# Kernel optimization log

Measured on AMD Instinct MI355X. Metric: run time of the kernel, lower is better.

The kernel has to match this reference:

```python
import jax, jax.numpy as jnp
import numpy as np

B, C, H, W = 8, 512, 64, 64
WS, NH = 8, 16
HD = C // NH
SCALE = float(HD) ** -0.5
L = WS * WS  # tokens per window
BN_EPS = 1e-5


def _rel_index():
    # Swin relative position index, (L, L) int table into (2*WS-1)^2 bias rows
    ch = np.arange(WS)
    coords = np.stack(np.meshgrid(ch, ch, indexing='ij'))  # (2, WS, WS)
    cf = coords.reshape(2, -1)
    rel = cf[:, :, None] - cf[:, None, :]
    rel = rel.transpose(1, 2, 0).copy()
    rel[:, :, 0] += WS - 1
    rel[:, :, 1] += WS - 1
    rel[:, :, 0] *= 2 * WS - 1
    return jnp.asarray(rel.sum(-1))

REL_IDX = _rel_index()


def conv2d(x, w, pad=0, groups=1):
    return jax.lax.conv_general_dilated(
        x, w, (1, 1), [(pad, pad), (pad, pad)],
        feature_group_count=groups,
        dimension_numbers=('NCHW', 'OIHW', 'NCHW'))


def bn(x, g, b):
    # eval-mode BatchNorm with running_mean=0, running_var=1 (fresh init)
    inv = 1.0 / np.sqrt(1.0 + BN_EPS)
    return g[None, :, None, None] * (x * inv) + b[None, :, None, None]


def avgpool(x, kh, kw, ph, pw):
    # torch AvgPool2d: zero padding, count_include_pad=True
    s = jax.lax.reduce_window(x, 0.0, jax.lax.add, (1, 1, kh, kw), (1, 1, 1, 1),
                              ((0, 0), (0, 0), (ph, ph), (pw, pw)))
    return s / (kh * kw)


def setup_inputs() -> dict:
    key = jax.random.key(0)
    ks = jax.random.split(key, 8)
    r = lambda k, s: jax.random.normal(k, s, dtype=jnp.float32) * 0.02
    return {
        'x': jax.random.normal(ks[0], (B, C, H, W), dtype=jnp.float32),
        'w_lc1': r(ks[1], (C, C, 1, 1)),
        'g1': jnp.ones((C,), jnp.float32), 'b1': jnp.zeros((C,), jnp.float32),
        'w_lc2': r(ks[2], (C, C, 3, 3)),
        'g2': jnp.ones((C,), jnp.float32), 'b2': jnp.zeros((C,), jnp.float32),
        'w_qkv': r(ks[3], (3 * C, C, 1, 1)),
        'rel_table': r(ks[4], ((2 * WS - 1) * (2 * WS - 1), NH)),
        'w_dw': r(ks[5], (C, 1, WS, WS)),
        'g3': jnp.ones((C,), jnp.float32), 'b3': jnp.zeros((C,), jnp.float32),
        'w_pw': r(ks[6], (C, C, 1, 1)),
    }


def reference(x, w_lc1, g1, b1, w_lc2, g2, b2, w_qkv, rel_table, w_dw, g3, b3, w_pw):
    # local branch: 1x1 conv+BN  +  3x3 conv+BN
    local = bn(conv2d(x, w_lc1), g1, b1) + bn(conv2d(x, w_lc2, pad=1), g2, b2)

    # H, W divisible by WS -> pad() is a no-op; Hp, Wp = H, W
    hh, ww = H // WS, W // WS
    qkv = conv2d(x, w_qkv)  # (B, 3C, H, W)
    # 'b (qkv h d) (hh ws1) (ww ws2) -> qkv (b hh ww) h (ws1 ws2) d'
    qkv = qkv.reshape(B, 3, NH, HD, hh, WS, ww, WS)
    qkv = qkv.transpose(1, 0, 4, 6, 2, 5, 7, 3).reshape(3, B * hh * ww, NH, L, HD)
    q, k, v = qkv[0], qkv[1], qkv[2]

    dots = jnp.einsum('bhid,bhjd->bhij', q, k) * SCALE  # (Bw, NH, L, L)
    bias = rel_table[REL_IDX]                            # (L, L, NH)
    dots = dots + bias.transpose(2, 0, 1)[None]
    attn = jax.nn.softmax(dots, axis=-1)
    out = jnp.einsum('bhij,bhjd->bhid', attn, v)         # (Bw, NH, L, HD)

    # '(b hh ww) h (ws1 ws2) d -> b (h d) (hh ws1) (ww ws2)'
    out = out.reshape(B, hh, ww, NH, WS, WS, HD)
    out = out.transpose(0, 3, 6, 1, 4, 2, 5).reshape(B, C, H, W)

    ax = avgpool(jnp.pad(out, ((0, 0), (0, 0), (0, 1), (0, 0)), mode='reflect'),
                 WS, 1, WS // 2 - 1, 0)
    ay = avgpool(jnp.pad(out, ((0, 0), (0, 0), (0, 0), (0, 1)), mode='reflect'),
                 1, WS, 0, WS // 2 - 1)
    out = ax + ay + local

    # pad_out + SeparableConvBN(kernel=WS): depthwise conv -> BN -> 1x1 conv
    out = jnp.pad(out, ((0, 0), (0, 0), (0, 1), (0, 1)), mode='reflect')
    out = conv2d(out, w_dw, pad=(WS - 1) // 2, groups=C)
    out = bn(out, g3, b3)
    out = conv2d(out, w_pw)
    return out[:, :, :H, :W]
```

## Files before the change

kernel.cpp:

```cpp
#include <hip/hip_runtime.h>

#define INVBN 0.9999950000374997f
#define ATT_SCALE 0.17677669529663687f

typedef short bf16x8 __attribute__((ext_vector_type(8)));
typedef float f32x4  __attribute__((ext_vector_type(4)));
typedef unsigned short us8v __attribute__((ext_vector_type(8)));

#define AS1C(p) ((const __attribute__((address_space(1))) void*)(p))
#define AS3(p)  ((__attribute__((address_space(3))) void*)(p))

__device__ __forceinline__ float bf2f(unsigned short u) {
    return __uint_as_float(((unsigned)u) << 16);
}
__device__ __forceinline__ unsigned short f2bf(float f) {
    unsigned u = __float_as_uint(f);
    u += 0x7FFFu + ((u >> 16) & 1u);
    return (unsigned short)(u >> 16);
}

__global__ __launch_bounds__(256)
void repack_kernel(const float* __restrict__ W2, const float* __restrict__ W1,
                   const float* __restrict__ Wq, const float* __restrict__ Wp,
                   const float* __restrict__ g1, const float* __restrict__ g2,
                   const float* __restrict__ b1, const float* __restrict__ b2,
                   unsigned short* __restrict__ Wt, unsigned short* __restrict__ WqO,
                   unsigned short* __restrict__ WpO, float* __restrict__ bsum)
{
    int i = blockIdx.x * 256 + threadIdx.x;
    if (i < 512) bsum[i] = b1[i] + b2[i];
    if (i < 786432) WqO[i] = f2bf(Wq[i]);
    if (i < 262144) WpO[i] = f2bf(Wp[i]);
    if (i >= 2359296) return;
    int tap = i / 262144;
    int rem = i - tap * 262144;
    int m   = rem >> 9;
    float v = g2[m] * INVBN * W2[(size_t)rem * 9 + tap];
    if (tap == 4) v = fmaf(g1[m] * INVBN, W1[rem], v);
    Wt[i] = f2bf(v);
}

__global__ __launch_bounds__(256)
void bias_precompute_kernel(const float* __restrict__ RT, float* __restrict__ biasM)
{
    int idx = blockIdx.x * 256 + threadIdx.x;
    int h = idx >> 10, rem = idx & 1023;
    int frag = rem >> 6, lane = rem & 63;
    int fi = frag >> 2, fj = frag & 3;
    int q  = 16 * fj + (lane & 15);
    int kb = 16 * fi + ((lane >> 4) << 2);
    int yi = q >> 3, xi = q & 7;
    float4 o;
    float* op = (float*)&o;
#pragma unroll
    for (int r = 0; r < 4; ++r) {
        int j = kb + r;
        int ridx = (yi - (j >> 3) + 7) * 15 + (xi - (j & 7) + 7);
        op[r] = RT[ridx * 16 + h];
    }
    *(float4*)&biasM[(size_t)idx * 4] = o;
}

__global__ __launch_bounds__(256)
void pad_transpose_kernel(const float* __restrict__ X, unsigned short* __restrict__ XT)
{
    int ph = blockIdx.x;
    int b  = blockIdx.y;
    int t  = threadIdx.x;
    unsigned short* rowbase = XT + ((size_t)b * 4356 + (size_t)ph * 66) * 512;
    uint4 z = make_uint4(0, 0, 0, 0);
    if (ph == 0 || ph == 65) {
        uint4* p4 = (uint4*)rowbase;
        for (int i = t; i < 4224; i += 256) p4[i] = z;
        return;
    }
    if (t < 64)       ((uint4*)rowbase)[t] = z;
    else if (t < 128) ((uint4*)(rowbase + 65 * 512))[t - 64] = z;

    int h = ph - 1;
    __shared__ float tile[64][65];
    const float* xb = X + (size_t)b * 512 * 4096 + h * 64;
    for (int cc = 0; cc < 8; ++cc) {
        int c0 = cc * 64;
        __syncthreads();
#pragma unroll
        for (int i = 0; i < 4; ++i) {
            int cl = i * 16 + (t >> 4);
            int w0 = (t & 15) * 4;
            *(float4*)&tile[cl][w0] =
                *(const float4*)&xb[(size_t)(c0 + cl) * 4096 + w0];
        }
        __syncthreads();
#pragma unroll
        for (int it = 0; it < 2; ++it) {
            int wl = it * 32 + (t >> 3);
            int cs = (t & 7) * 8;
            us8v v;
#pragma unroll
            for (int e = 0; e < 8; ++e) v[e] = f2bf(tile[cs + e][wl]);
            *(us8v*)&rowbase[(size_t)(1 + wl) * 512 + c0 + cs] = v;
        }
    }
}

template<int NTAPS, bool PAD, typename OT>
__global__ __launch_bounds__(256)
void mfma_gemm(const unsigned short* __restrict__ A,
               const unsigned short* __restrict__ Bw,
               const float* __restrict__ bias,
               OT* __restrict__ Out, int M)
{
    __shared__ short As[128 * 64];
    __shared__ short Bs[128 * 64];

    const int t  = threadIdx.x;
    const int n0 = blockIdx.x * 128;
    const int m0 = blockIdx.y * 128;
    const int b  = blockIdx.z;
    const unsigned short* Ab = A + (size_t)b * (PAD ? 4356 * 512 : 4096 * 512);
    OT* Ob = Out + (size_t)b * ((size_t)M * 4096);

    const int trow = t >> 3;
    const int csrc = (t & 7) ^ (trow & 7);
    const unsigned short* aSrc[4];
    const unsigned short* bSrc[4];
#pragma unroll
    for (int i = 0; i < 4; ++i) {
        int r = i * 32 + trow;
        int p = n0 + r;
        if (PAD) {
            int h = p >> 6, w = p & 63;
            aSrc[i] = Ab + ((size_t)((h + 1) * 66 + (w + 1)) * 512 + csrc * 8);
        } else {
            aSrc[i] = Ab + ((size_t)p * 512 + csrc * 8);
        }
        bSrc[i] = Bw + ((size_t)(m0 + r) * 512 + csrc * 8);
    }
    short* aDst = As + (t & 192) * 8;
    short* bDst = Bs + (t & 192) * 8;

    const int lane = t & 63;
    const int wv = t >> 6, wr = wv >> 1, wc = wv & 1;
    const int lrow = lane & 15, lk = lane >> 4;
    int aOff[4][2], bOff[4][2];
#pragma unroll
    for (int f = 0; f < 4; ++f)
#pragma unroll
        for (int kk = 0; kk < 2; ++kk) {
            int ra = wr * 64 + f * 16 + lrow;
            aOff[f][kk] = ra * 64 + ((kk * 4 + lk) ^ (ra & 7)) * 8;
            int rb = wc * 64 + f * 16 + lrow;
            bOff[f][kk] = rb * 64 + ((kk * 4 + lk) ^ (rb & 7)) * 8;
        }

    f32x4 acc[4][4] = {};

#pragma unroll 1
    for (int tap = 0; tap < NTAPS; ++tap) {
        const int dr  = (NTAPS == 9) ? (tap / 3 - 1) : 0;
        const int dsh = (NTAPS == 9) ? (tap % 3 - 1) : 0;
        const int aTapOff = (dr * 66 + dsh) * 512;
        const size_t bTapOff = (size_t)tap * (size_t)M * 512;
#pragma unroll 1
        for (int ks = 0; ks < 8; ++ks) {
            const int k0 = ks * 64;
            __syncthreads();
#pragma unroll
            for (int i = 0; i < 4; ++i) {
                __builtin_amdgcn_global_load_lds(
                    AS1C(aSrc[i] + aTapOff + k0), AS3(aDst + i * 2048), 16, 0, 0);
                __builtin_amdgcn_global_load_lds(
                    AS1C(bSrc[i] + bTapOff + k0), AS3(bDst + i * 2048), 16, 0, 0);
            }
            __syncthreads();
            bf16x8 av[4][2], bv[4][2];
#pragma unroll
            for (int f = 0; f < 4; ++f) {
                av[f][0] = *(const bf16x8*)&As[aOff[f][0]];
                av[f][1] = *(const bf16x8*)&As[aOff[f][1]];
                bv[f][0] = *(const bf16x8*)&Bs[bOff[f][0]];
                bv[f][1] = *(const bf16x8*)&Bs[bOff[f][1]];
            }
#pragma unroll
            for (int kk = 0; kk < 2; ++kk)
#pragma unroll
                for (int fn = 0; fn < 4; ++fn)
#pragma unroll
                    for (int fm = 0; fm < 4; ++fm)
                        acc[fn][fm] = __builtin_amdgcn_mfma_f32_16x16x32_bf16(
                            av[fn][kk], bv[fm][kk], acc[fn][fm], 0, 0, 0);
        }
    }

#pragma unroll
    for (int fm = 0; fm < 4; ++fm) {
        int m = m0 + wc * 64 + fm * 16 + lrow;
        float bv = bias ? bias[m] : 0.f;
        size_t mrow = (size_t)m * 4096;
#pragma unroll
        for (int fn = 0; fn < 4; ++fn) {
            int nb = n0 + wr * 64 + fn * 16 + lk * 4;
            f32x4 a4 = acc[fn][fm];
            if constexpr (sizeof(OT) == 2) {
                ushort4 o;
                o.x = f2bf(a4[0] + bv);
                o.y = f2bf(a4[1] + bv);
                o.z = f2bf(a4[2] + bv);
                o.w = f2bf(a4[3] + bv);
                *(ushort4*)&Ob[mrow + nb] = o;
            } else {
                *(float4*)&Ob[mrow + nb] =
                    make_float4(a4[0] + bv, a4[1] + bv, a4[2] + bv, a4[3] + bv);
            }
        }
    }
}

__global__ __launch_bounds__(256)
void attn_mfma_kernel(const unsigned short* __restrict__ QKV,
                      const float* __restrict__ biasM,
                      float* __restrict__ OutB)
{
    __shared__ short smem[4 * 9216];
    int t = threadIdx.x;
    int wv = t >> 6, lane = t & 63;
    int wing = blockIdx.x >> 2;
    int head = (blockIdx.x & 3) * 4 + wv;
    int b    = blockIdx.y;
    int hhi = wing >> 3, wwi = wing & 7;
    int sp0 = hhi * 512 + wwi * 8;
    int ch0 = head * 32;
    const unsigned short* Qg = QKV + (size_t)b * 1536 * 4096;

    short* Qtm = smem + wv * 9216;
    short* Ktm = Qtm + 2304;
    short* Pq  = Qtm + 4608;

    {
        int d  = lane & 31;
        int rb = lane >> 5;
#pragma unroll
        for (int i = 0; i < 4; ++i) {
            int r = rb + 2 * i;
            us8v q8 = *(const us8v*)&Qg[(size_t)(ch0 + d) * 4096 + sp0 + r * 64];
            us8v k8 = *(const us8v*)&Qg[(size_t)(512 + ch0 + d) * 4096 + sp0 + r * 64];
#pragma unroll
            for (int e = 0; e < 8; ++e) {
                Qtm[(r * 8 + e) * 36 + d] = (short)q8[e];
                Ktm[(r * 8 + e) * 36 + d] = (short)k8[e];
            }
        }
    }

    int lrow = lane & 15, lk = lane >> 4;

    bf16x8 kf[4], qf[4];
#pragma unroll
    for (int f = 0; f < 4; ++f) {
        kf[f] = *(const bf16x8*)&Ktm[(lrow + 16 * f) * 36 + lk * 8];
        qf[f] = *(const bf16x8*)&Qtm[(lrow + 16 * f) * 36 + lk * 8];
    }
    f32x4 s[4][4] = {};
#pragma unroll
    for (int fi = 0; fi < 4; ++fi)
#pragma unroll
        for (int fj = 0; fj < 4; ++fj)
            s[fi][fj] = __builtin_amdgcn_mfma_f32_16x16x32_bf16(
                kf[fi], qf[fj], s[fi][fj], 0, 0, 0);

    const float* bM = biasM + (size_t)head * 4096;
    float rs[4];
#pragma unroll
    for (int fj = 0; fj < 4; ++fj) {
        float v[4][4];
#pragma unroll
        for (int fi = 0; fi < 4; ++fi) {
            float4 bv = *(const float4*)&bM[((fi * 4 + fj) * 64 + lane) * 4];
            const float* bvp = (const float*)&bv;
#pragma unroll
            for (int r = 0; r < 4; ++r)
                v[fi][r] = fmaf(s[fi][fj][r], ATT_SCALE, bvp[r]);
        }
        float m = -1e30f;
#pragma unroll
        for (int fi = 0; fi < 4; ++fi)
#pragma unroll
            for (int r = 0; r < 4; ++r) m = fmaxf(m, v[fi][r]);
        m = fmaxf(m, __shfl_xor(m, 16));
        m = fmaxf(m, __shfl_xor(m, 32));
        float ev[4][4];
        float sum = 0.f;
#pragma unroll
        for (int fi = 0; fi < 4; ++fi)
#pragma unroll
            for (int r = 0; r < 4; ++r) {
                ev[fi][r] = __expf(v[fi][r] - m);
                sum += ev[fi][r];
            }
        sum += __shfl_xor(sum, 16);
        sum += __shfl_xor(sum, 32);
        rs[fj] = 1.f / sum;
#pragma unroll
        for (int fi = 0; fi < 4; ++fi) {
            unsigned p0 = (unsigned)f2bf(ev[fi][0]) | ((unsigned)f2bf(ev[fi][1]) << 16);
            unsigned p1 = (unsigned)f2bf(ev[fi][2]) | ((unsigned)f2bf(ev[fi][3]) << 16);
            *(uint2*)&Pq[(lrow + 16 * fj) * 72 + 16 * fi + lk * 4] = make_uint2(p0, p1);
        }
    }

    f32x4 o[2][4] = {};
#pragma unroll
    for (int ks = 0; ks < 2; ++ks) {
        bf16x8 vf[2], pf[4];
#pragma unroll
        for (int fid = 0; fid < 2; ++fid)
            vf[fid] = *(const bf16x8*)&Qg[(size_t)(1024 + ch0 + 16 * fid + lrow) * 4096
                                          + sp0 + (lk + 4 * ks) * 64];
#pragma unroll
        for (int fjq = 0; fjq < 4; ++fjq)
            pf[fjq] = *(const bf16x8*)&Pq[(lrow + 16 * fjq) * 72 + ks * 32 + lk * 8];
#pragma unroll
        for (int fid = 0; fid < 2; ++fid)
#pragma unroll
            for (int fjq = 0; fjq < 4; ++fjq)
                o[fid][fjq] = __builtin_amdgcn_mfma_f32_16x16x32_bf16(
                    vf[fid], pf[fjq], o[fid][fjq], 0, 0, 0);
    }

    float* Out = OutB + (size_t)b * 512 * 4096;
#pragma unroll
    for (int fjq = 0; fjq < 4; ++fjq) {
        int q  = lrow + 16 * fjq;
        int sp = sp0 + ((q >> 3) << 6) + (q & 7);
        float rr = rs[fjq];
#pragma unroll
        for (int fid = 0; fid < 2; ++fid)
#pragma unroll
            for (int r = 0; r < 4; ++r) {
                int dch = 16 * fid + lk * 4 + r;
                Out[(size_t)(ch0 + dch) * 4096 + sp] = o[fid][fjq][r] * rr;
            }
    }
}

__global__ __launch_bounds__(256)
void pooldw_kernel(const float* __restrict__ A, const unsigned short* __restrict__ L,
                   const float* __restrict__ Wd,
                   const float* __restrict__ g3, const float* __restrict__ b3,
                   unsigned short* __restrict__ U)
{
    int bc = blockIdx.x;
    int c  = bc & 511;
    __shared__ float pad[72][72];
    int t = threadIdx.x;
    float* pf = &pad[0][0];
#pragma unroll
    for (int i = 0; i < 21; ++i) {
        int e = i * 256 + t;
        if (e < 5184) pf[e] = 0.f;
    }
    __syncthreads();

    const float* ap = A + (size_t)bc * 4096;
#pragma unroll
    for (int i = 0; i < 4; ++i) {
        int idx = i * 256 + t;
        int y = idx >> 4, x4 = (idx & 15) * 4;
        *(float4*)&pad[3 + y][4 + x4] = ((const float4*)ap)[idx];
    }
    if (t < 64)       pad[67][4 + t] = ap[62 * 64 + t];
    else if (t < 128) { int y = t - 64; pad[3 + y][68] = ap[y * 64 + 62]; }
    else if (t == 128) pad[67][68] = ap[62 * 64 + 62];
    __syncthreads();

    const unsigned short* lp = L + (size_t)bc * 4096;
    int u  = t & 15, rr = t >> 4;
    int w0 = u * 4;
    float4 res[4];
#pragma unroll
    for (int g = 0; g < 4; ++g) {
        int h = g * 16 + rr;
        float4 sx = make_float4(0.f, 0.f, 0.f, 0.f);
#pragma unroll
        for (int i = 0; i < 8; ++i) {
            float4 v = *(const float4*)&pad[h + i][4 + w0];
            sx.x += v.x; sx.y += v.y; sx.z += v.z; sx.w += v.w;
        }
        float win[12];
        *(float4*)&win[0] = *(const float4*)&pad[3 + h][w0];
        *(float4*)&win[4] = *(const float4*)&pad[3 + h][w0 + 4];
        *(float4*)&win[8] = *(const float4*)&pad[3 + h][w0 + 8];
        float4 sy = make_float4(0.f, 0.f, 0.f, 0.f);
#pragma unroll
        for (int i = 0; i < 8; ++i) {
            sy.x += win[1 + i];
            sy.y += win[2 + i];
            sy.z += win[3 + i];
            sy.w += win[4 + i];
        }
        ushort4 l4 = *(const ushort4*)&lp[h * 64 + w0];
        res[g].x = fmaf(0.125f, sx.x + sy.x, bf2f(l4.x));
        res[g].y = fmaf(0.125f, sx.y + sy.y, bf2f(l4.y));
        res[g].z = fmaf(0.125f, sx.z + sy.z, bf2f(l4.z));
        res[g].w = fmaf(0.125f, sx.w + sy.w, bf2f(l4.w));
    }
    __syncthreads();

#pragma unroll
    for (int g = 0; g < 4; ++g) {
        int h = g * 16 + rr;
        *(float4*)&pad[3 + h][4 + w0] = res[g];
    }
    __syncthreads();
    if (t < 64)       pad[67][4 + t] = pad[65][4 + t];
    else if (t < 128) { int y = t - 64; pad[3 + y][68] = pad[3 + y][66]; }
    else if (t == 128) pad[67][68] = pad[65][66];
    __syncthreads();

    const float* wdp = Wd + c * 64;
    float gc  = g3[c] * INVBN;
    float bcv = b3[c];
#pragma unroll
    for (int g = 0; g < 4; ++g) {
        int h = g * 16 + rr;
        float a0 = 0.f, a1 = 0.f, a2 = 0.f, a3 = 0.f;
#pragma unroll
        for (int i = 0; i < 8; ++i) {
            float win[12];
            *(float4*)&win[0] = *(const float4*)&pad[h + i][w0];
            *(float4*)&win[4] = *(const float4*)&pad[h + i][w0 + 4];
            *(float4*)&win[8] = *(const float4*)&pad[h + i][w0 + 8];
#pragma unroll
            for (int j = 0; j < 8; ++j) {
                float wv = wdp[i * 8 + j];
                a0 = fmaf(wv, win[1 + j], a0);
                a1 = fmaf(wv, win[2 + j], a1);
                a2 = fmaf(wv, win[3 + j], a2);
                a3 = fmaf(wv, win[4 + j], a3);
            }
        }
        ushort4 o;
        o.x = f2bf(gc * a0 + bcv);
        o.y = f2bf(gc * a1 + bcv);
        o.z = f2bf(gc * a2 + bcv);
        o.w = f2bf(gc * a3 + bcv);
        *(ushort4*)&U[(size_t)bc * 4096 + h * 64 + w0] = o;
    }
}

__global__ __launch_bounds__(256)
void transpose_cp_kernel(const unsigned short* __restrict__ U, unsigned short* __restrict__ Ut)
{
    int pt = blockIdx.x;
    int b  = blockIdx.y;
    const unsigned short* Ub = U + (size_t)b * 512 * 4096;
    unsigned short* Utb = Ut + (size_t)b * 4096 * 512;
    __shared__ unsigned short tile[64][72];
    int t = threadIdx.x;
    int p0 = pt * 64;

    for (int cc = 0; cc < 8; ++cc) {
        int c0 = cc * 64;
        __syncthreads();
        {
            int cl = t >> 2, px = (t & 3) * 16;
            const unsigned short* src = &Ub[(size_t)(c0 + cl) * 4096 + p0 + px];
            *(us8v*)&tile[cl][px]     = *(const us8v*)src;
            *(us8v*)&tile[cl][px + 8] = *(const us8v*)(src + 8);
        }
        __syncthreads();
        {
            int pl = t >> 2, cx = (t & 3) * 16;
            us8v o0, o1;
#pragma unroll
            for (int e = 0; e < 8; ++e) {
                o0[e] = tile[cx + e][pl];
                o1[e] = tile[cx + 8 + e][pl];
            }
            unsigned short* dst = &Utb[(size_t)(p0 + pl) * 512 + c0 + cx];
            *(us8v*)dst       = o0;
            *(us8v*)(dst + 8) = o1;
        }
    }
}

extern "C" void kernel_launch(void* const* d_in, const int* in_sizes, int n_in,
                              void* d_out, int out_size, void* d_ws, size_t ws_size,
                              hipStream_t stream)
{
    (void)in_sizes; (void)n_in; (void)out_size;
    const float* x     = (const float*)d_in[0];
    const float* w_lc1 = (const float*)d_in[1];
    const float* g1    = (const float*)d_in[2];
    const float* b1    = (const float*)d_in[3];
    const float* w_lc2 = (const float*)d_in[4];
    const float* g2    = (const float*)d_in[5];
    const float* b2    = (const float*)d_in[6];
    const float* w_qkv = (const float*)d_in[7];
    const float* rt    = (const float*)d_in[8];
    const float* w_dw  = (const float*)d_in[9];
    const float* g3    = (const float*)d_in[10];
    const float* b3    = (const float*)d_in[11];
    const float* w_pw  = (const float*)d_in[12];
    float* out = (float*)d_out;

    unsigned short* S        = (unsigned short*)d_ws;
    unsigned short* local_us = S;
    unsigned short* xt_us    = S + 16777216;
    unsigned short* u_us     = xt_us;
    unsigned short* wt3_us   = S + 34619392;
    unsigned short* wq_us    = S + 36978688;
    unsigned short* wpw_us   = S + 37765120;
    float*          bsum     = (float*)(S + 38027264);
    float*          biasM    = (float*)(S + 38028288);
    unsigned short* qkv_us   = S + 38552576;
    unsigned short* ut_us    = local_us;

    const bool full = ws_size >= (size_t)(38552576 + 50331648) * 2;

    repack_kernel<<<dim3(9216), 256, 0, stream>>>(w_lc2, w_lc1, w_qkv, w_pw,
                                                  g1, g2, b1, b2,
                                                  wt3_us, wq_us, wpw_us, bsum);
    bias_precompute_kernel<<<dim3(64), 256, 0, stream>>>(rt, biasM);
    pad_transpose_kernel<<<dim3(66, 8), 256, 0, stream>>>(x, xt_us);
    mfma_gemm<9, true, unsigned short><<<dim3(32, 4, 8), 256, 0, stream>>>(
        xt_us, wt3_us, bsum, local_us, 512);

    if (full) {
        mfma_gemm<1, true, unsigned short><<<dim3(32, 12, 8), 256, 0, stream>>>(
            xt_us, wq_us, nullptr, qkv_us, 1536);
        attn_mfma_kernel<<<dim3(256, 8), 256, 0, stream>>>(qkv_us, biasM, out);
    } else {
        for (int b = 0; b < 8; ++b) {
            mfma_gemm<1, true, unsigned short><<<dim3(32, 12, 1), 256, 0, stream>>>(
                xt_us + (size_t)b * 4356 * 512, wq_us, nullptr, qkv_us, 1536);
            attn_mfma_kernel<<<dim3(256, 1), 256, 0, stream>>>(
                qkv_us, biasM, out + (size_t)b * 2097152);
        }
    }

    pooldw_kernel<<<dim3(4096), 256, 0, stream>>>(out, local_us, w_dw, g3, b3, u_us);
    transpose_cp_kernel<<<dim3(64, 8), 256, 0, stream>>>(u_us, ut_us);
    mfma_gemm<1, false, float><<<dim3(32, 4, 8), 256, 0, stream>>>(
        ut_us, wpw_us, nullptr, out, 512);
}
```

Baseline: 513.8 us.

## Use 256x256-tile multistage pipelined MFMA GEMM for conv3x3 and QKV projections

Adds a new GEMM kernel with 512 threads per block and a 256x256 output tile. It keeps a 4-buffer LDS ring filled by direct global-to-LDS loads, waits on vmcnt counters before each barrier so loads overlap MFMA compute, and raises wave priority around the MFMA bursts. The 3x3 local conv and the QKV projection now use it instead of the 128x128 single-buffered GEMM, which synchronised twice per K step. The old kernel is kept only for the f32-output pointwise GEMM. In exchange each block takes up to 128KB of LDS, which limits occupancy, and the unswizzled 32-wide LDS rows may cause bank conflicts.

Measured after the change: 475.9 us. 1.08x faster.

```diff
diff --git a/kernel.cpp b/kernel.cpp
--- a/kernel.cpp
+++ b/kernel.cpp
@@ -9,6 +9,10 @@
 
 #define AS1C(p) ((const __attribute__((address_space(1))) void*)(p))
 #define AS3(p)  ((__attribute__((address_space(3))) void*)(p))
+
+#define VMCNT_BARRIER(Nstr) do {                                   \
+    asm volatile("s_waitcnt vmcnt(" Nstr ")" ::: "memory");        \
+    __builtin_amdgcn_s_barrier(); } while (0)
 
 __device__ __forceinline__ float bf2f(unsigned short u) {
     return __uint_as_float(((unsigned)u) << 16);
@@ -103,12 +107,122 @@
     }
 }
 
-template<int NTAPS, bool PAD, typename OT>
+template<int NTAPS>
+__global__ __launch_bounds__(512, 2)
+void mfma_gemm256(const unsigned short* __restrict__ A,
+                  const unsigned short* __restrict__ Bw,
+                  const float* __restrict__ bias,
+                  unsigned short* __restrict__ Out, int M)
+{
+    __shared__ __align__(16) unsigned short ldsbuf[65536];
+
+    const int t    = threadIdx.x;
+    const int wid  = t >> 6, lane = t & 63;
+    const int wr   = wid >> 2, wc = wid & 3;
+    const int lrow = lane & 15, lk = lane >> 4;
+    const int n0 = blockIdx.x * 256;
+    const int m0 = blockIdx.y * 256;
+    const int b  = blockIdx.z;
+    const unsigned short* Ab = A + (size_t)b * (4356 * 512);
+    unsigned short* Ob = Out + (size_t)b * ((size_t)M * 4096);
+
+    const unsigned short* src[4];
+    {
+        int rsub = lane >> 2, ch = lane & 3;
+#pragma unroll
+        for (int i = 0; i < 4; ++i) {
+            if (wid < 4) {
+                int p = n0 + (wid * 4 + i) * 16 + rsub;
+                int h = p >> 6, w = p & 63;
+                src[i] = Ab + (size_t)((h + 1) * 66 + (w + 1)) * 512 + ch * 8;
+            } else {
+                int m = m0 + ((wid - 4) * 4 + i) * 16 + rsub;
+                src[i] = Bw + (size_t)m * 512 + ch * 8;
+            }
+        }
+    }
+
+    f32x4 acc[8][4] = {};
+
+    auto aScal = [&](int tt) -> int {
+        if (NTAPS == 1) return tt * 32;
+        int tap = tt >> 4;
+        return (tap / 3 - 1) * (66 * 512) + (tap % 3 - 1) * 512 + (tt & 15) * 32;
+    };
+    auto bScal = [&](int tt) -> int {
+        if (NTAPS == 1) return tt * 32;
+        return (tt >> 4) * (M * 512) + (tt & 15) * 32;
+    };
+    auto STAGE = [&](int bufk, int aoff, int boff) {
+        int off = (wid < 4) ? aoff : boff;
+#pragma unroll
+        for (int i = 0; i < 4; ++i)
+            __builtin_amdgcn_global_load_lds(
+                AS1C(src[i] + off),
+                AS3(&ldsbuf[bufk * 16384 + (wid * 4 + i) * 512]), 16, 0, 0);
+    };
+    auto COMPUTE = [&](int bufk) {
+        const unsigned short* Ak = &ldsbuf[bufk * 16384];
+        const unsigned short* Bk = &ldsbuf[bufk * 16384 + 8192];
+        bf16x8 af[8], bfr[4];
+#pragma unroll
+        for (int f = 0; f < 8; ++f)
+            af[f] = *(const bf16x8*)&Ak[(wr * 128 + f * 16 + lrow) * 32 + lk * 8];
+#pragma unroll
+        for (int g = 0; g < 4; ++g)
+            bfr[g] = *(const bf16x8*)&Bk[(wc * 64 + g * 16 + lrow) * 32 + lk * 8];
+        __builtin_amdgcn_s_setprio(1);
+#pragma unroll
+        for (int f = 0; f < 8; ++f)
+#pragma unroll
+            for (int g = 0; g < 4; ++g)
+                acc[f][g] = __builtin_amdgcn_mfma_f32_16x16x32_bf16(
+                    af[f], bfr[g], acc[f][g], 0, 0, 0);
+        __builtin_amdgcn_s_setprio(0);
+    };
+
+    constexpr int NT = NTAPS * 16;
+
+    STAGE(0, aScal(0), bScal(0));
+    STAGE(1, aScal(1), bScal(1));
+    STAGE(2, aScal(2), bScal(2));
+    VMCNT_BARRIER("8");
+
+#pragma unroll 1
+    for (int tb = 0; tb < NT - 4; tb += 4) {
+        STAGE(3, aScal(tb + 3), bScal(tb + 3)); COMPUTE(0); VMCNT_BARRIER("8");
+        STAGE(0, aScal(tb + 4), bScal(tb + 4)); COMPUTE(1); VMCNT_BARRIER("8");
+        STAGE(1, aScal(tb + 5), bScal(tb + 5)); COMPUTE(2); VMCNT_BARRIER("8");
+        STAGE(2, aScal(tb + 6), bScal(tb + 6)); COMPUTE(3); VMCNT_BARRIER("8");
+    }
+    STAGE(3, aScal(NT - 1), bScal(NT - 1)); COMPUTE(0); VMCNT_BARRIER("8");
+    COMPUTE(1); VMCNT_BARRIER("4");
+    COMPUTE(2); VMCNT_BARRIER("0");
+    COMPUTE(3);
+
+#pragma unroll
+    for (int g = 0; g < 4; ++g) {
+        int m = m0 + wc * 64 + g * 16 + lrow;
+        float bv = bias ? bias[m] : 0.f;
+        size_t mrow = (size_t)m * 4096;
+#pragma unroll
+        for (int f = 0; f < 8; ++f) {
+            int nb = n0 + wr * 128 + f * 16 + lk * 4;
+            f32x4 a4 = acc[f][g];
+            ushort4 o;
+            o.x = f2bf(a4[0] + bv);
+            o.y = f2bf(a4[1] + bv);
+            o.z = f2bf(a4[2] + bv);
+            o.w = f2bf(a4[3] + bv);
+            *(ushort4*)&Ob[mrow + nb] = o;
+        }
+    }
+}
+
 __global__ __launch_bounds__(256)
-void mfma_gemm(const unsigned short* __restrict__ A,
-               const unsigned short* __restrict__ Bw,
-               const float* __restrict__ bias,
-               OT* __restrict__ Out, int M)
+void mfma_gemm_f32out(const unsigned short* __restrict__ A,
+                      const unsigned short* __restrict__ Bw,
+                      float* __restrict__ Out, int M)
 {
     __shared__ short As[128 * 64];
     __shared__ short Bs[128 * 64];
@@ -117,8 +231,8 @@
     const int n0 = blockIdx.x * 128;
     const int m0 = blockIdx.y * 128;
     const int b  = blockIdx.z;
-    const unsigned short* Ab = A + (size_t)b * (PAD ? 4356 * 512 : 4096 * 512);
-    OT* Ob = Out + (size_t)b * ((size_t)M * 4096);
+    const unsigned short* Ab = A + (size_t)b * (4096 * 512);
+    float* Ob = Out + (size_t)b * ((size_t)M * 4096);
 
     const int trow = t >> 3;
     const int csrc = (t & 7) ^ (trow & 7);
@@ -127,13 +241,7 @@
 #pragma unroll
     for (int i = 0; i < 4; ++i) {
         int r = i * 32 + trow;
-        int p = n0 + r;
-        if (PAD) {
-            int h = p >> 6, w = p & 63;
-            aSrc[i] = Ab + ((size_t)((h + 1) * 66 + (w + 1)) * 512 + csrc * 8);
-        } else {
-            aSrc[i] = Ab + ((size_t)p * 512 + csrc * 8);
-        }
+        aSrc[i] = Ab + ((size_t)(n0 + r) * 512 + csrc * 8);
         bSrc[i] = Bw + ((size_t)(m0 + r) * 512 + csrc * 8);
     }
     short* aDst = As + (t & 192) * 8;
@@ -156,62 +264,44 @@
     f32x4 acc[4][4] = {};
 
 #pragma unroll 1
-    for (int tap = 0; tap < NTAPS; ++tap) {
-        const int dr  = (NTAPS == 9) ? (tap / 3 - 1) : 0;
-        const int dsh = (NTAPS == 9) ? (tap % 3 - 1) : 0;
-        const int aTapOff = (dr * 66 + dsh) * 512;
-        const size_t bTapOff = (size_t)tap * (size_t)M * 512;
-#pragma unroll 1
-        for (int ks = 0; ks < 8; ++ks) {
-            const int k0 = ks * 64;
-            __syncthreads();
-#pragma unroll
-            for (int i = 0; i < 4; ++i) {
-                __builtin_amdgcn_global_load_lds(
-                    AS1C(aSrc[i] + aTapOff + k0), AS3(aDst + i * 2048), 16, 0, 0);
-                __builtin_amdgcn_global_load_lds(
-                    AS1C(bSrc[i] + bTapOff + k0), AS3(bDst + i * 2048), 16, 0, 0);
-            }
-            __syncthreads();
-            bf16x8 av[4][2], bv[4][2];
-#pragma unroll
-            for (int f = 0; f < 4; ++f) {
-                av[f][0] = *(const bf16x8*)&As[aOff[f][0]];
-                av[f][1] = *(const bf16x8*)&As[aOff[f][1]];
-                bv[f][0] = *(const bf16x8*)&Bs[bOff[f][0]];
-                bv[f][1] = *(const bf16x8*)&Bs[bOff[f][1]];
-            }
-#pragma unroll
-            for (int kk = 0; kk < 2; ++kk)
-#pragma unroll
-                for (int fn = 0; fn < 4; ++fn)
-#pragma unroll
-                    for (int fm = 0; fm < 4; ++fm)
-                        acc[fn][fm] = __builtin_amdgcn_mfma_f32_16x16x32_bf16(
-                            av[fn][kk], bv[fm][kk], acc[fn][fm], 0, 0, 0);
-        }
+    for (int ks = 0; ks < 8; ++ks) {
+        const int k0 = ks * 64;
+        __syncthreads();
+#pragma unroll
+        for (int i = 0; i < 4; ++i) {
+            __builtin_amdgcn_global_load_lds(
+                AS1C(aSrc[i] + k0), AS3(aDst + i * 2048), 16, 0, 0);
+            __builtin_amdgcn_global_load_lds(
+                AS1C(bSrc[i] + k0), AS3(bDst + i * 2048), 16, 0, 0);
+        }
+        __syncthreads();
+        bf16x8 av[4][2], bv[4][2];
+#pragma unroll
+        for (int f = 0; f < 4; ++f) {
+            av[f][0] = *(const bf16x8*)&As[aOff[f][0]];
+            av[f][1] = *(const bf16x8*)&As[aOff[f][1]];
+            bv[f][0] = *(const bf16x8*)&Bs[bOff[f][0]];
+            bv[f][1] = *(const bf16x8*)&Bs[bOff[f][1]];
+        }
+#pragma unroll
+        for (int kk = 0; kk < 2; ++kk)
+#pragma unroll
+            for (int fn = 0; fn < 4; ++fn)
+#pragma unroll
+                for (int fm = 0; fm < 4; ++fm)
+                    acc[fn][fm] = __builtin_amdgcn_mfma_f32_16x16x32_bf16(
+                        av[fn][kk], bv[fm][kk], acc[fn][fm], 0, 0, 0);
     }
 
 #pragma unroll
     for (int fm = 0; fm < 4; ++fm) {
         int m = m0 + wc * 64 + fm * 16 + lrow;
-        float bv = bias ? bias[m] : 0.f;
         size_t mrow = (size_t)m * 4096;
 #pragma unroll
         for (int fn = 0; fn < 4; ++fn) {
             int nb = n0 + wr * 64 + fn * 16 + lk * 4;
             f32x4 a4 = acc[fn][fm];
-            if constexpr (sizeof(OT) == 2) {
-                ushort4 o;
-                o.x = f2bf(a4[0] + bv);
-                o.y = f2bf(a4[1] + bv);
-                o.z = f2bf(a4[2] + bv);
-                o.w = f2bf(a4[3] + bv);
-                *(ushort4*)&Ob[mrow + nb] = o;
-            } else {
-                *(float4*)&Ob[mrow + nb] =
-                    make_float4(a4[0] + bv, a4[1] + bv, a4[2] + bv, a4[3] + bv);
-            }
+            *(float4*)&Ob[mrow + nb] = make_float4(a4[0], a4[1], a4[2], a4[3]);
         }
     }
 }
@@ -523,16 +613,16 @@
                                                   wt3_us, wq_us, wpw_us, bsum);
     bias_precompute_kernel<<<dim3(64), 256, 0, stream>>>(rt, biasM);
     pad_transpose_kernel<<<dim3(66, 8), 256, 0, stream>>>(x, xt_us);
-    mfma_gemm<9, true, unsigned short><<<dim3(32, 4, 8), 256, 0, stream>>>(
+    mfma_gemm256<9><<<dim3(16, 2, 8), 512, 0, stream>>>(
         xt_us, wt3_us, bsum, local_us, 512);
 
     if (full) {
-        mfma_gemm<1, true, unsigned short><<<dim3(32, 12, 8), 256, 0, stream>>>(
+        mfma_gemm256<1><<<dim3(16, 6, 8), 512, 0, stream>>>(
             xt_us, wq_us, nullptr, qkv_us, 1536);
         attn_mfma_kernel<<<dim3(256, 8), 256, 0, stream>>>(qkv_us, biasM, out);
     } else {
         for (int b = 0; b < 8; ++b) {
-            mfma_gemm<1, true, unsigned short><<<dim3(32, 12, 1), 256, 0, stream>>>(
+            mfma_gemm256<1><<<dim3(16, 6, 1), 512, 0, stream>>>(
                 xt_us + (size_t)b * 4356 * 512, wq_us, nullptr, qkv_us, 1536);
             attn_mfma_kernel<<<dim3(256, 1), 256, 0, stream>>>(
                 qkv_us, biasM, out + (size_t)b * 2097152);
@@ -541,6 +631,6 @@
 
     pooldw_kernel<<<dim3(4096), 256, 0, stream>>>(out, local_us, w_dw, g3, b3, u_us);
     transpose_cp_kernel<<<dim3(64, 8), 256, 0, stream>>>(u_us, ut_us);
-    mfma_gemm<1, false, float><<<dim3(32, 4, 8), 256, 0, stream>>>(
-        ut_us, wpw_us, nullptr, out, 512);
-}
+    mfma_gemm_f32out<<<dim3(32, 4, 8), 256, 0, stream>>>(
+        ut_us, wpw_us, out, 512);
+}
```
